# Optimization experiments

Measured on AMD Instinct MI355X. Metric: run time of the kernel, lower is better.

The kernel has to match this reference:

```python
import jax, jax.numpy as jnp
import numpy as np

B, CIN, COUT, H, W, K = 16, 16, 16, 256, 256, 3


def setup_inputs() -> dict:
    key = jax.random.key(0)
    k1, k2, k3 = jax.random.split(key, 3)
    x = jax.random.normal(k1, (B, CIN, H, W), dtype=jnp.float32)
    # complex weights stored as two real tensors (out, in, k, k)
    w_real = jax.random.normal(k2, (COUT, CIN, K, K), dtype=jnp.float32)
    w_imag = jax.random.normal(k3, (COUT, CIN, K, K), dtype=jnp.float32)
    return {"x": x, "w_real": w_real, "w_imag": w_imag}


def reference(x, w_real, w_imag):
    # x: (B, Cin, H, W) real; weights: (Cout, Cin, K, K) complex (as two reals)
    Cout, Cin, k, _ = w_real.shape
    h, w = x.shape[-2], x.shape[-1]
    wc = (w_real + 1j * w_imag).astype(jnp.complex64)
    # zero-pad kernel to (Cout, Cin, H, W); batch dim in the original is redundant
    kp = jnp.zeros((Cout, Cin, h, w), dtype=jnp.complex64).at[:, :, :k, :k].set(wc)
    kernel_freq = jnp.fft.fft2(kp)  # (Cout, Cin, H, W) complex
    # out_freq = x.unsqueeze(1) * kernel_freq; sum over in_channels -> (B, Cout, H, W)
    out = jnp.einsum('bihw,oihw->bohw', x.astype(jnp.complex64), kernel_freq)
    # return complex result as stacked (real, imag): shape (2, B, Cout, H, W)
    return jnp.stack([out.real, out.imag])
```

## Files before the change

### kernel.cpp

```cpp
#include <hip/hip_runtime.h>


typedef _Float16 half4 __attribute__((ext_vector_type(4)));
typedef float floatx4 __attribute__((ext_vector_type(4)));

constexpr int Hd = 256, Wd = 256;
constexpr int TW = 16;
constexpr float TWO_PI = 6.283185307179586f;

__global__ __launch_bounds__(256)
void build_G(const float* __restrict__ wr, const float* __restrict__ wi,
             float* __restrict__ G) {
    const int w = blockIdx.x;
    const int t = threadIdx.x;
    const int o = t >> 4, i = t & 15;
    float s1, c1;
    __sincosf((TWO_PI / 256.f) * (float)w, &s1, &c1);
    const float ewr[3] = {1.f, c1, c1 * c1 - s1 * s1};
    const float ewi[3] = {0.f, -s1, -2.f * s1 * c1};
    const float* a = &wr[(o * 16 + i) * 9];
    const float* b = &wi[(o * 16 + i) * 9];
#pragma unroll
    for (int p = 0; p < 3; ++p) {
        float gr = 0.f, gi = 0.f;
#pragma unroll
        for (int q = 0; q < 3; ++q) {
            const float A = a[p * 3 + q], B = b[p * 3 + q];
            gr += A * ewr[q] - B * ewi[q];
            gi += A * ewi[q] + B * ewr[q];
        }
        reinterpret_cast<float2*>(G)[(w * 3 + p) * 256 + o * 16 + i] =
            make_float2(gr, gi);
    }
}

__global__ __launch_bounds__(512)
void freq_conv_mfma(const float* __restrict__ x, const float* __restrict__ G,
                    float* __restrict__ out) {
    __shared__ float XS[TW * 256];
    __shared__ float CB[2 * 256 * 20];

    const int tid  = threadIdx.x;
    const int bid  = blockIdx.x;
    const int h    = bid >> 4;
    const int w0   = (bid & 15) * TW;
    const int lane = tid & 63;
    const int wave = tid >> 6;
    const int nlo  = lane & 15;
    const int hi   = lane >> 4;

#pragma unroll
    for (int k = 0; k < 2; ++k) {
        const int idx = k * 512 + tid;
        const int r   = idx >> 2;
        const int c   = idx & 3;
        const float4 v = *reinterpret_cast<const float4*>(
            &x[(size_t)r * (Hd * Wd) + h * Wd + w0 + 4 * c]);
        const int rr = (r + 4 * c) & 255;
        XS[(4 * c + 0) * 256 + rr] = v.x;
        XS[(4 * c + 1) * 256 + rr] = v.y;
        XS[(4 * c + 2) * 256 + rr] = v.z;
        XS[(4 * c + 3) * 256 + rr] = v.w;
    }

    float s1, c1;
    __sincosf((TWO_PI / 256.f) * (float)h, &s1, &c1);
    const float ehr[3] = {1.f, c1, c1 * c1 - s1 * s1};
    const float ehi[3] = {0.f, -s1, -2.f * s1 * c1};

    __syncthreads();

#pragma unroll
    for (int kk = 0; kk < 2; ++kk) {
        const int wl = kk * 8 + wave;
        const int w  = w0 + wl;

        const float4 xa = *reinterpret_cast<const float4*>(
            &XS[wl * 256 + (((nlo * 16 + 4 * hi) + 4 * (wl >> 2)) & 255)]);
        const half4 Af = {(_Float16)xa.x, (_Float16)xa.y,
                          (_Float16)xa.z, (_Float16)xa.w};

        float Kr[4] = {0.f, 0.f, 0.f, 0.f}, Ki[4] = {0.f, 0.f, 0.f, 0.f};
#pragma unroll
        for (int p = 0; p < 3; ++p) {
            const float* gp = &G[((w * 3 + p) * 256 + nlo * 16 + 4 * hi) * 2];
            const float4 g0 = *reinterpret_cast<const float4*>(gp);
            const float4 g1 = *reinterpret_cast<const float4*>(gp + 4);
            const float er = ehr[p], ei = ehi[p];
            Kr[0] += er * g0.x - ei * g0.y;  Ki[0] += er * g0.y + ei * g0.x;
            Kr[1] += er * g0.z - ei * g0.w;  Ki[1] += er * g0.w + ei * g0.z;
            Kr[2] += er * g1.x - ei * g1.y;  Ki[2] += er * g1.y + ei * g1.x;
            Kr[3] += er * g1.z - ei * g1.w;  Ki[3] += er * g1.w + ei * g1.z;
        }
        const half4 Br = {(_Float16)Kr[0], (_Float16)Kr[1],
                          (_Float16)Kr[2], (_Float16)Kr[3]};
        const half4 Bi = {(_Float16)Ki[0], (_Float16)Ki[1],
                          (_Float16)Ki[2], (_Float16)Ki[3]};

        const floatx4 zero = {0.f, 0.f, 0.f, 0.f};
        const floatx4 Cr = __builtin_amdgcn_mfma_f32_16x16x16f16(Af, Br, zero, 0, 0, 0);
        const floatx4 Ci = __builtin_amdgcn_mfma_f32_16x16x16f16(Af, Bi, zero, 0, 0, 0);

        const int wsz = (wl + 4 * hi) & 15;
#pragma unroll
        for (int r = 0; r < 4; ++r) {
            const int row = (4 * hi + r) * 16 + nlo;
            CB[row * 20 + wsz]             = Cr[r];
            CB[256 * 20 + row * 20 + wsz]  = Ci[r];
        }
    }
    __syncthreads();

#pragma unroll
    for (int pass = 0; pass < 4; ++pass) {
        const int R  = pass * 128 + (tid >> 2);
        const int wp = tid & 3;
        const int b  = (R >> 4) & 15;
        const int wl_l = (4 * wp + 4 * (b >> 2)) & 15;
        const float4 v = *reinterpret_cast<const float4*>(
            &CB[(R >> 8) * (256 * 20) + (R & 255) * 20 + wl_l]);
        *reinterpret_cast<float4*>(
            &out[(size_t)R * (Hd * Wd) + h * Wd + w0 + 4 * wp]) = v;
    }
}

extern "C" void kernel_launch(void* const* d_in, const int* in_sizes, int n_in,
                              void* d_out, int out_size, void* d_ws, size_t ws_size,
                              hipStream_t stream) {
    const float* x  = (const float*)d_in[0];
    const float* wr = (const float*)d_in[1];
    const float* wi = (const float*)d_in[2];
    float* out = (float*)d_out;
    float* G   = (float*)d_ws;

    build_G<<<256, 256, 0, stream>>>(wr, wi, G);
    freq_conv_mfma<<<Hd * (Wd / TW), 512, 0, stream>>>(x, G, out);
}
```

Measured before the change: 231.5 us.

## Fuse kernel-spectrum build into conv kernel and tile sixteen rows per block

Removes the separate build_G launch. Each block now recomputes its W-partial kernel spectrum in shared memory as packed fp16 complex values, then loops over 16 rows of H, double-buffering fp16 x tiles in LDS and prefetching the next row into registers. The grid shrinks from 4096 blocks of 512 threads to 256 blocks of 1024 threads, which saves a launch and the global G reads in exchange for less parallelism and a barrier per row. G is now stored in fp16, which lowers precision slightly.

```diff
diff --git a/kernel.cpp b/kernel.cpp
--- a/kernel.cpp
+++ b/kernel.cpp
@@ -1,126 +1,158 @@
 #include <hip/hip_runtime.h>
 
 
-typedef _Float16 half4 __attribute__((ext_vector_type(4)));
-typedef float floatx4 __attribute__((ext_vector_type(4)));
+typedef _Float16 half2v __attribute__((ext_vector_type(2)));
+typedef _Float16 half4  __attribute__((ext_vector_type(4)));
+typedef float   floatx4 __attribute__((ext_vector_type(4)));
 
 constexpr int Hd = 256, Wd = 256;
 constexpr int TW = 16;
+constexpr int TH = 16;
+constexpr int NT = 1024;
+constexpr int XSS = 280;
 constexpr float TWO_PI = 6.283185307179586f;
+constexpr size_t IMAG_OFF = (size_t)16 * 16 * Hd * Wd;
 
-__global__ __launch_bounds__(256)
-void build_G(const float* __restrict__ wr, const float* __restrict__ wi,
-             float* __restrict__ G) {
-    const int w = blockIdx.x;
-    const int t = threadIdx.x;
-    const int o = t >> 4, i = t & 15;
-    float s1, c1;
-    __sincosf((TWO_PI / 256.f) * (float)w, &s1, &c1);
-    const float ewr[3] = {1.f, c1, c1 * c1 - s1 * s1};
-    const float ewi[3] = {0.f, -s1, -2.f * s1 * c1};
-    const float* a = &wr[(o * 16 + i) * 9];
-    const float* b = &wi[(o * 16 + i) * 9];
-#pragma unroll
-    for (int p = 0; p < 3; ++p) {
-        float gr = 0.f, gi = 0.f;
-#pragma unroll
-        for (int q = 0; q < 3; ++q) {
-            const float A = a[p * 3 + q], B = b[p * 3 + q];
-            gr += A * ewr[q] - B * ewi[q];
-            gi += A * ewi[q] + B * ewr[q];
-        }
-        reinterpret_cast<float2*>(G)[(w * 3 + p) * 256 + o * 16 + i] =
-            make_float2(gr, gi);
-    }
-}
-
-__global__ __launch_bounds__(512)
-void freq_conv_mfma(const float* __restrict__ x, const float* __restrict__ G,
-                    float* __restrict__ out) {
-    __shared__ float XS[TW * 256];
-    __shared__ float CB[2 * 256 * 20];
+__global__ __launch_bounds__(NT)
+void freq_conv(const float* __restrict__ x,
+               const float* __restrict__ wr_g,
+               const float* __restrict__ wi_g,
+               float* __restrict__ out)
+{
+    __shared__ __align__(16) unsigned int Gs[TW * 3 * 256];
+    __shared__ __align__(16) _Float16 XS[2][TW * XSS];
+    __shared__ __align__(16) float CB[2 * 256 * 20];
 
     const int tid  = threadIdx.x;
-    const int bid  = blockIdx.x;
-    const int h    = bid >> 4;
-    const int w0   = (bid & 15) * TW;
     const int lane = tid & 63;
     const int wave = tid >> 6;
     const int nlo  = lane & 15;
     const int hi   = lane >> 4;
 
+    const int bid = blockIdx.x;
+    const int h0  = (bid >> 4) * TH;
+    const int w0  = (bid & 15) * TW;
+
+    const int xrow = tid >> 2;
+    const int xwg  = tid & 3;
+    float4 xr = *reinterpret_cast<const float4*>(
+        &x[(size_t)xrow * (Hd * Wd) + (size_t)h0 * Wd + w0 + 4 * xwg]);
+
+    {
+        float* WS = CB;
+        if (tid < 576) {
+            reinterpret_cast<float4*>(WS)[tid] =
+                reinterpret_cast<const float4*>(wr_g)[tid];
+        } else {
+            reinterpret_cast<float4*>(WS + 2304)[tid - 576] =
+                reinterpret_cast<const float4*>(wi_g)[tid - 576];
+        }
+        if (tid < 128) {
+            reinterpret_cast<float4*>(WS + 2304)[448 + tid] =
+                reinterpret_cast<const float4*>(wi_g)[448 + tid];
+        }
+    }
+    __syncthreads();
+
+    {
+        const float* Wr = CB;
+        const float* Wi = CB + 2304;
+        const int oi = tid & 255;
+        const int g  = tid >> 8;
+        float a[9], b9[9];
 #pragma unroll
-    for (int k = 0; k < 2; ++k) {
-        const int idx = k * 512 + tid;
-        const int r   = idx >> 2;
-        const int c   = idx & 3;
-        const float4 v = *reinterpret_cast<const float4*>(
-            &x[(size_t)r * (Hd * Wd) + h * Wd + w0 + 4 * c]);
-        const int rr = (r + 4 * c) & 255;
-        XS[(4 * c + 0) * 256 + rr] = v.x;
-        XS[(4 * c + 1) * 256 + rr] = v.y;
-        XS[(4 * c + 2) * 256 + rr] = v.z;
-        XS[(4 * c + 3) * 256 + rr] = v.w;
+        for (int t = 0; t < 9; ++t) { a[t] = Wr[oi * 9 + t]; b9[t] = Wi[oi * 9 + t]; }
+#pragma unroll
+        for (int k = 0; k < 4; ++k) {
+            const int wl = g + 4 * k;
+            float s1, c1;
+            __sincosf((TWO_PI / 256.f) * (float)(w0 + wl), &s1, &c1);
+            const float cw[3] = {1.f, c1, c1 * c1 - s1 * s1};
+            const float sw[3] = {0.f, s1, 2.f * s1 * c1};
+#pragma unroll
+            for (int p = 0; p < 3; ++p) {
+                float gr = 0.f, gi = 0.f;
+#pragma unroll
+                for (int q = 0; q < 3; ++q) {
+                    gr += a[p * 3 + q] * cw[q] + b9[p * 3 + q] * sw[q];
+                    gi += b9[p * 3 + q] * cw[q] - a[p * 3 + q] * sw[q];
+                }
+                half2v hv = {(_Float16)gr, (_Float16)gi};
+                Gs[(wl * 3 + p) * 256 + oi] = __builtin_bit_cast(unsigned int, hv);
+            }
+        }
     }
 
-    float s1, c1;
-    __sincosf((TWO_PI / 256.f) * (float)h, &s1, &c1);
-    const float ehr[3] = {1.f, c1, c1 * c1 - s1 * s1};
-    const float ehi[3] = {0.f, -s1, -2.f * s1 * c1};
+    {
+#pragma unroll
+        for (int j = 0; j < 4; ++j)
+            XS[0][(4 * xwg + j) * XSS + xrow] = (_Float16)((&xr.x)[j]);
+    }
+    xr = *reinterpret_cast<const float4*>(
+        &x[(size_t)xrow * (Hd * Wd) + (size_t)(h0 + 1) * Wd + w0 + 4 * xwg]);
 
-    __syncthreads();
+    for (int ih = 0; ih < TH; ++ih) {
+        const int h = h0 + ih;
+        __syncthreads();
 
+        if (ih + 1 < TH) {
 #pragma unroll
-    for (int kk = 0; kk < 2; ++kk) {
-        const int wl = kk * 8 + wave;
-        const int w  = w0 + wl;
+            for (int j = 0; j < 4; ++j)
+                XS[(ih + 1) & 1][(4 * xwg + j) * XSS + xrow] = (_Float16)((&xr.x)[j]);
+            if (ih + 2 < TH)
+                xr = *reinterpret_cast<const float4*>(
+                    &x[(size_t)xrow * (Hd * Wd) + (size_t)(h + 2) * Wd + w0 + 4 * xwg]);
+        }
 
-        const float4 xa = *reinterpret_cast<const float4*>(
-            &XS[wl * 256 + (((nlo * 16 + 4 * hi) + 4 * (wl >> 2)) & 255)]);
-        const half4 Af = {(_Float16)xa.x, (_Float16)xa.y,
-                          (_Float16)xa.z, (_Float16)xa.w};
+        float s1, c1;
+        __sincosf((TWO_PI / 256.f) * (float)h, &s1, &c1);
+        const float chv[3] = {1.f, c1, c1 * c1 - s1 * s1};
+        const float shv[3] = {0.f, s1, 2.f * s1 * c1};
 
+        const int wl = wave;
         float Kr[4] = {0.f, 0.f, 0.f, 0.f}, Ki[4] = {0.f, 0.f, 0.f, 0.f};
 #pragma unroll
         for (int p = 0; p < 3; ++p) {
-            const float* gp = &G[((w * 3 + p) * 256 + nlo * 16 + 4 * hi) * 2];
-            const float4 g0 = *reinterpret_cast<const float4*>(gp);
-            const float4 g1 = *reinterpret_cast<const float4*>(gp + 4);
-            const float er = ehr[p], ei = ehi[p];
-            Kr[0] += er * g0.x - ei * g0.y;  Ki[0] += er * g0.y + ei * g0.x;
-            Kr[1] += er * g0.z - ei * g0.w;  Ki[1] += er * g0.w + ei * g0.z;
-            Kr[2] += er * g1.x - ei * g1.y;  Ki[2] += er * g1.y + ei * g1.x;
-            Kr[3] += er * g1.z - ei * g1.w;  Ki[3] += er * g1.w + ei * g1.z;
+            const uint4 g4 = *reinterpret_cast<const uint4*>(
+                &Gs[(wl * 3 + p) * 256 + nlo * 16 + 4 * hi]);
+            const float er = chv[p], ei = shv[p];
+            const unsigned int gw[4] = {g4.x, g4.y, g4.z, g4.w};
+#pragma unroll
+            for (int j = 0; j < 4; ++j) {
+                const half2v gv = __builtin_bit_cast(half2v, gw[j]);
+                const float gr = (float)gv.x, gi = (float)gv.y;
+                Kr[j] += er * gr + ei * gi;
+                Ki[j] += er * gi - ei * gr;
+            }
         }
         const half4 Br = {(_Float16)Kr[0], (_Float16)Kr[1],
                           (_Float16)Kr[2], (_Float16)Kr[3]};
         const half4 Bi = {(_Float16)Ki[0], (_Float16)Ki[1],
                           (_Float16)Ki[2], (_Float16)Ki[3]};
+        const half4 Af = *reinterpret_cast<const half4*>(
+            &XS[ih & 1][wl * XSS + nlo * 16 + 4 * hi]);
 
         const floatx4 zero = {0.f, 0.f, 0.f, 0.f};
         const floatx4 Cr = __builtin_amdgcn_mfma_f32_16x16x16f16(Af, Br, zero, 0, 0, 0);
         const floatx4 Ci = __builtin_amdgcn_mfma_f32_16x16x16f16(Af, Bi, zero, 0, 0, 0);
-
-        const int wsz = (wl + 4 * hi) & 15;
 #pragma unroll
         for (int r = 0; r < 4; ++r) {
             const int row = (4 * hi + r) * 16 + nlo;
-            CB[row * 20 + wsz]             = Cr[r];
-            CB[256 * 20 + row * 20 + wsz]  = Ci[r];
+            CB[row * 20 + wl]         = Cr[r];
+            CB[(256 + row) * 20 + wl] = Ci[r];
         }
-    }
-    __syncthreads();
 
-#pragma unroll
-    for (int pass = 0; pass < 4; ++pass) {
-        const int R  = pass * 128 + (tid >> 2);
-        const int wp = tid & 3;
-        const int b  = (R >> 4) & 15;
-        const int wl_l = (4 * wp + 4 * (b >> 2)) & 15;
-        const float4 v = *reinterpret_cast<const float4*>(
-            &CB[(R >> 8) * (256 * 20) + (R & 255) * 20 + wl_l]);
-        *reinterpret_cast<float4*>(
-            &out[(size_t)R * (Hd * Wd) + h * Wd + w0 + 4 * wp]) = v;
+        __syncthreads();
+
+        {
+            const int row4 = tid >> 2;
+            const int wp   = tid & 3;
+            const float4 v0 = *reinterpret_cast<const float4*>(&CB[row4 * 20 + 4 * wp]);
+            const float4 v1 = *reinterpret_cast<const float4*>(&CB[(256 + row4) * 20 + 4 * wp]);
+            float* o0 = &out[(size_t)row4 * (Hd * Wd) + (size_t)h * Wd + w0 + 4 * wp];
+            *reinterpret_cast<float4*>(o0) = v0;
+            *reinterpret_cast<float4*>(o0 + IMAG_OFF) = v1;
+        }
     }
 }
 
@@ -131,8 +163,6 @@
     const float* wr = (const float*)d_in[1];
     const float* wi = (const float*)d_in[2];
     float* out = (float*)d_out;
-    float* G   = (float*)d_ws;
 
-    build_G<<<256, 256, 0, stream>>>(wr, wi, G);
-    freq_conv_mfma<<<Hd * (Wd / TW), 512, 0, stream>>>(x, G, out);
+    freq_conv<<<dim3(256), dim3(NT), 0, stream>>>(x, wr, wi, out);
 }
```

New measurement: 207.7 us. 10.2% less time.
